# Optimization experiments

Hardware: AMD Instinct MI355X
Metric: run time of the kernel (lower is better)

The kernel has to match this reference:

```python
import math
import jax, jax.numpy as jnp
import numpy as np

NUM_BUCKETS = 32
MAX_DISTANCE = 128
N_HEADS = 16
D_KV = 64


def _relative_position_bucket(rel_pos, num_buckets=NUM_BUCKETS, max_distance=MAX_DISTANCE):
    # bidirectional=True branch of T5's bucketing
    num_buckets = num_buckets // 2
    rel_buckets = (rel_pos > 0).astype(jnp.int32) * num_buckets
    rel_pos = jnp.abs(rel_pos)
    max_exact = num_buckets // 2
    is_small = rel_pos < max_exact
    # safe log (values < max_exact are masked out by is_small)
    rp_f = jnp.maximum(rel_pos, 1).astype(jnp.float32)
    rel_if_large = max_exact + (
        jnp.log(rp_f / max_exact) / math.log(max_distance / max_exact) * (num_buckets - max_exact)
    ).astype(jnp.int32)
    rel_if_large = jnp.minimum(rel_if_large, num_buckets - 1)
    return rel_buckets + jnp.where(is_small, rel_pos, rel_if_large)


def compute_bias(rel_bias_table, q_len, k_len):
    ctx = jnp.arange(q_len)[:, None]
    mem = jnp.arange(k_len)[None, :]
    buckets = _relative_position_bucket(mem - ctx)  # [q, k]
    values = rel_bias_table[buckets]                # [q, k, h]
    return jnp.transpose(values, (2, 0, 1))[None]   # [1, h, q, k]


def setup_inputs() -> dict:
    key = jax.random.key(0)
    k1, k2, k3, k4 = jax.random.split(key, 4)
    d_model = 1024
    return {
        "hidden_states": jax.random.normal(k1, (2, 2048, d_model), jnp.float32),
        "w_qkv": jax.random.normal(k2, (d_model, 3 * N_HEADS * D_KV), jnp.float32) * (d_model ** -0.5),
        "w_o": jax.random.normal(k3, (N_HEADS * D_KV, d_model), jnp.float32) * ((N_HEADS * D_KV) ** -0.5),
        "rel_bias_table": jax.random.normal(k4, (NUM_BUCKETS, N_HEADS), jnp.float32),
    }


def reference(hidden_states, w_qkv, w_o, rel_bias_table):
    b, s, _ = hidden_states.shape
    inner = N_HEADS * D_KV
    qkv = hidden_states @ w_qkv                         # [b, s, 3*inner]
    q, k, v = jnp.split(qkv, [inner, 2 * inner], axis=-1)
    def to_bhsd(x):
        return jnp.transpose(x.reshape(b, s, N_HEADS, D_KV), (0, 2, 1, 3))
    q, k, v = to_bhsd(q), to_bhsd(k), to_bhsd(v)
    scores = jnp.einsum("bhqd,bhkd->bhqk", q, k)        # no 1/sqrt(d) scaling in T5
    position_bias = compute_bias(rel_bias_table, s, s)  # [1, h, q, k]
    scores = scores + position_bias
    attn = jax.nn.softmax(scores.astype(jnp.float32), axis=-1).astype(scores.dtype)
    out = jnp.einsum("bhqk,bhkd->bhqd", attn, v)
    out = jnp.transpose(out, (0, 2, 1, 3)).reshape(b, s, inner)
    attn_output = out @ w_o
    return attn_output, position_bias
```

## Files before the change

kernel.cpp:

```cpp
#include <hip/hip_runtime.h>
#include <hip/hip_bf16.h>
#include <cstdint>
#include <cstddef>

#define S_LEN 2048
#define NH 16
#define DKV 64
#define BATCH 2
#define DMODEL 1024
#define LOG2E 1.4426950408889634f

typedef _Float16 half_t;
typedef __attribute__((ext_vector_type(4))) _Float16 halfx4;
typedef __attribute__((ext_vector_type(8))) _Float16 half8;
typedef __attribute__((ext_vector_type(4))) float floatx4;

__device__ __forceinline__ void load_lds16(const half_t* g, half_t* l) {
  __builtin_amdgcn_global_load_lds((const __attribute__((address_space(1))) void*)g,
                                   (__attribute__((address_space(3))) void*)l, 16, 0, 0);
}

__device__ __forceinline__ int t5_bucket(int delta) {
  int base = (delta > 0) ? 16 : 0;
  int a = delta < 0 ? -delta : delta;
  int n;
  if (a < 8)       n = a;
  else if (a < 12) n = 8;
  else if (a < 16) n = 9;
  else if (a < 23) n = 10;
  else if (a < 32) n = 11;
  else if (a < 46) n = 12;
  else if (a < 64) n = 13;
  else if (a < 91) n = 14;
  else             n = 15;
  return base + n;
}

__global__ __launch_bounds__(256) void bias_kernel(const float* __restrict__ table,
                                                   float* __restrict__ out) {
  int h = blockIdx.x >> 11;
  int q = blockIdx.x & (S_LEN - 1);
  __shared__ float tb[32];
  if (threadIdx.x < 32) tb[threadIdx.x] = table[threadIdx.x * NH + h];
  __syncthreads();
  float* dst = out + (size_t)blockIdx.x * S_LEN;
  int k0 = threadIdx.x * 4;
#pragma unroll
  for (int half = 0; half < 2; half++) {
    int k = k0 + half * 1024;
    float4 v;
    v.x = tb[t5_bucket((k + 0) - q)];
    v.y = tb[t5_bucket((k + 1) - q)];
    v.z = tb[t5_bucket((k + 2) - q)];
    v.w = tb[t5_bucket((k + 3) - q)];
    *(float4*)(dst + k) = v;
  }
}

__global__ __launch_bounds__(256) void cast_f2h(const float* __restrict__ in,
                                                half_t* __restrict__ out) {
  int i = blockIdx.x * 256 + threadIdx.x;
  float4 v = ((const float4*)in)[i];
  halfx4 h;
  h[0] = (half_t)v.x; h[1] = (half_t)v.y; h[2] = (half_t)v.z; h[3] = (half_t)v.w;
  ((halfx4*)out)[i] = h;
}

__global__ __launch_bounds__(256) void transpose_cast(const float* __restrict__ in,
                                                      half_t* __restrict__ out,
                                                      int R, int C) {
  __shared__ float t[32][33];
  int lr = threadIdx.x >> 3;
  int lc = (threadIdx.x & 7) * 4;
  int r0 = blockIdx.y * 32, c0 = blockIdx.x * 32;
  float4 v = *(const float4*)(in + (size_t)(r0 + lr) * C + c0 + lc);
  t[lr][lc + 0] = v.x; t[lr][lc + 1] = v.y; t[lr][lc + 2] = v.z; t[lr][lc + 3] = v.w;
  __syncthreads();
  halfx4 hv;
#pragma unroll
  for (int u = 0; u < 4; u++) hv[u] = (half_t)t[lc + u][lr];
  *(halfx4*)(out + (size_t)(c0 + lr) * R + r0 + lc) = hv;
}

__global__ __launch_bounds__(256) void vtrans(const half_t* __restrict__ V,
                                              half_t* __restrict__ Vt) {
  __shared__ half_t T[64 * 72];
  const int bh = blockIdx.y;
  const int s0 = blockIdx.x * 64;
  const half_t* src = V + ((size_t)bh * S_LEN + s0) * DKV;
  half_t* dst = Vt + (size_t)bh * DKV * S_LEN + s0;
  const int sr = threadIdx.x >> 3;
  const int dc = (threadIdx.x & 7) * 8;
#pragma unroll
  for (int p = 0; p < 2; p++) {
    int s = sr + p * 32;
    half8 v = *(const half8*)(src + (size_t)s * DKV + dc);
#pragma unroll
    for (int u = 0; u < 8; u++) T[(dc + u) * 72 + s] = v[u];
  }
  __syncthreads();
#pragma unroll
  for (int p = 0; p < 2; p++) {
    int d = sr + p * 32;
    half8 v = *(half8*)&T[d * 72 + dc];
    *(half8*)(dst + (size_t)d * S_LEN + dc) = v;
  }
}

template <int MODE>
__global__ __launch_bounds__(256) void hgemm128(const half_t* __restrict__ A,
                                                const half_t* __restrict__ Bt,
                                                float* __restrict__ C,
                                                half_t* __restrict__ Qo,
                                                half_t* __restrict__ Ko,
                                                half_t* __restrict__ Vo,
                                                int M, int N, int K) {
  __shared__ half_t Asl[8 * 512];
  __shared__ half_t Bsl[8 * 512];

  const int tid = threadIdx.x;
  const int w = tid >> 6;
  const int lane = tid & 63;
  const int l15 = lane & 15;
  const int quad = lane >> 4;
  const int wm = w >> 1, wn = w & 1;
  const int m0 = blockIdx.y * 128;
  const int n0 = blockIdx.x * 128;

  floatx4 acc[4][4];
#pragma unroll
  for (int i = 0; i < 4; i++)
#pragma unroll
    for (int j = 0; j < 4; j++) acc[i][j] = (floatx4){0.f, 0.f, 0.f, 0.f};

  const half_t* ga0 = A + (size_t)(m0 + (2 * w + 0) * 16 + l15) * K + quad * 8;
  const half_t* ga1 = A + (size_t)(m0 + (2 * w + 1) * 16 + l15) * K + quad * 8;
  const half_t* gb0 = Bt + (size_t)(n0 + (2 * w + 0) * 16 + l15) * K + quad * 8;
  const half_t* gb1 = Bt + (size_t)(n0 + (2 * w + 1) * 16 + l15) * K + quad * 8;
  half_t* la0 = &Asl[(2 * w + 0) * 512];
  half_t* la1 = &Asl[(2 * w + 1) * 512];
  half_t* lb0 = &Bsl[(2 * w + 0) * 512];
  half_t* lb1 = &Bsl[(2 * w + 1) * 512];

  for (int k0 = 0; k0 < K; k0 += 32) {
    __syncthreads();
    load_lds16(ga0 + k0, la0);
    load_lds16(ga1 + k0, la1);
    load_lds16(gb0 + k0, lb0);
    load_lds16(gb1 + k0, lb1);
    __syncthreads();

    half8 af[4], bf[4];
#pragma unroll
    for (int i = 0; i < 4; i++) af[i] = *(half8*)&Asl[(wm * 4 + i) * 512 + lane * 8];
#pragma unroll
    for (int j = 0; j < 4; j++) bf[j] = *(half8*)&Bsl[(wn * 4 + j) * 512 + lane * 8];
#pragma unroll
    for (int i = 0; i < 4; i++)
#pragma unroll
      for (int j = 0; j < 4; j++)
        acc[i][j] = __builtin_amdgcn_mfma_f32_16x16x32_f16(af[i], bf[j], acc[i][j], 0, 0, 0);
  }

  const int rowbase = m0 + wm * 64;
  const int colbase = n0 + wn * 64;
  if (MODE == 0) {
#pragma unroll
    for (int i = 0; i < 4; i++)
#pragma unroll
      for (int j = 0; j < 4; j++)
#pragma unroll
        for (int r = 0; r < 4; r++)
          C[(size_t)(rowbase + i * 16 + quad * 4 + r) * N + colbase + j * 16 + l15] =
              acc[i][j][r];
  } else {
    const int which = colbase >> 10;
    const int h = (colbase & 1023) >> 6;
    const int b = rowbase >> 11;
    const int s0 = rowbase & (S_LEN - 1);
    const float scale = (which == 0) ? LOG2E : 1.0f;
    half_t* base = ((which == 0) ? Qo : (which == 1) ? Ko : Vo) +
                   (size_t)(b * NH + h) * S_LEN * DKV;
#pragma unroll
    for (int i = 0; i < 4; i++)
#pragma unroll
      for (int j = 0; j < 4; j++)
#pragma unroll
        for (int r = 0; r < 4; r++)
          base[(size_t)(s0 + i * 16 + quad * 4 + r) * DKV + j * 16 + l15] =
              (half_t)(acc[i][j][r] * scale);
  }
}

__global__ __launch_bounds__(512) void attn_fused(const half_t* __restrict__ Q,
                                                  const half_t* __restrict__ K,
                                                  const half_t* __restrict__ Vt,
                                                  const float* __restrict__ table,
                                                  half_t* __restrict__ X) {
  __shared__ half_t Ks[64 * 64];
  __shared__ half_t Vts[64 * 64];
  __shared__ float tb[32];
  __shared__ float badd[184];

  const int tid = threadIdx.x;
  const int w = tid >> 6;
  const int lane = tid & 63;
  const int l15 = lane & 15;
  const int quad = lane >> 4;
  const int bh = blockIdx.y;
  const int h = bh & (NH - 1);
  const int q0w = blockIdx.x * 128 + w * 16;

  if (tid < 32) tb[tid] = table[tid * NH + h] * LOG2E;
  __syncthreads();
  if (tid < 183) badd[tid] = tb[t5_bucket(tid - 91)];
  const float tb_neg = tb[15], tb_pos = tb[31];

  half8 qf[2];
#pragma unroll
  for (int ks = 0; ks < 2; ks++)
    qf[ks] = *(const half8*)(Q + ((size_t)bh * S_LEN + q0w + l15) * DKV +
                             ks * 32 + quad * 8);

  floatx4 o[4];
#pragma unroll
  for (int nb = 0; nb < 4; nb++) o[nb] = (floatx4){0.f, 0.f, 0.f, 0.f};
  float m = -1e30f, l = 0.0f;

  const int jr = tid >> 3;
  const int u = tid & 7;
  const int swu = (u ^ (jr & 7)) * 8;
  const int kv_rd0 = l15 * 64 + ((0 * 4 + quad) ^ (l15 & 7)) * 8;
  const int kv_rd1 = l15 * 64 + ((1 * 4 + quad) ^ (l15 & 7)) * 8;
  const int q2h = quad >> 1, q2l = (quad & 1) * 4;

  const half_t* Kg = K + ((size_t)bh * S_LEN + jr) * DKV + u * 8;
  const half_t* Vg = Vt + ((size_t)bh * DKV + jr) * S_LEN + u * 8;
  int rel = -q0w;

  half8 kreg = *(const half8*)Kg;
  half8 vreg = *(const half8*)Vg;

  for (int it = 0; it < 32; it++, rel += 64) {
    __syncthreads();
    *(half8*)&Ks[jr * 64 + swu] = kreg;
    *(half8*)&Vts[jr * 64 + swu] = vreg;
    __syncthreads();
    if (it < 31) {
      Kg += 64 * DKV;
      Vg += 64;
      kreg = *(const half8*)Kg;
      vreg = *(const half8*)Vg;
    }

    floatx4 s[4];
#pragma unroll
    for (int nb = 0; nb < 4; nb++) {
      s[nb] = (floatx4){0.f, 0.f, 0.f, 0.f};
      s[nb] = __builtin_amdgcn_mfma_f32_16x16x32_f16(
          *(half8*)&Ks[nb * 1024 + kv_rd0], qf[0], s[nb], 0, 0, 0);
      s[nb] = __builtin_amdgcn_mfma_f32_16x16x32_f16(
          *(half8*)&Ks[nb * 1024 + kv_rd1], qf[1], s[nb], 0, 0, 0);
    }

    float cm = fmaxf(fmaxf(fmaxf(s[0][0], s[0][1]), fmaxf(s[0][2], s[0][3])),
                     fmaxf(fmaxf(s[1][0], s[1][1]), fmaxf(s[1][2], s[1][3])));
    cm = fmaxf(cm, fmaxf(fmaxf(fmaxf(s[2][0], s[2][1]), fmaxf(s[2][2], s[2][3])),
                         fmaxf(fmaxf(s[3][0], s[3][1]), fmaxf(s[3][2], s[3][3]))));
    {
      int i = __builtin_amdgcn_ds_swizzle(__float_as_int(cm), 0x401F);
      cm = fmaxf(cm, __int_as_float(i));
      cm = fmaxf(cm, __shfl_xor(cm, 32));
    }
    float mn = fmaxf(m, cm);
    if (!__all(cm <= m)) {
      float al = exp2f(m - mn);
      l *= al;
#pragma unroll
      for (int nb = 0; nb < 4; nb++)
#pragma unroll
        for (int r = 0; r < 4; r++) o[nb][r] *= al;
      m = mn;
    }

    float lsum = 0.0f;
    halfx4 pvb[4];
    if (rel >= 106 || rel <= -154) {
      const float sh = ((rel >= 106) ? tb_pos : tb_neg) - mn;
#pragma unroll
      for (int nb = 0; nb < 4; nb++)
#pragma unroll
        for (int r = 0; r < 4; r++) {
          float p = exp2f(s[nb][r] + sh);
          lsum += p;
          pvb[nb][r] = (half_t)p;
        }
    } else {
      const int db = rel + quad * 4 - l15 + 91;
#pragma unroll
      for (int nb = 0; nb < 4; nb++)
#pragma unroll
        for (int r = 0; r < 4; r++) {
          int idx = db + nb * 16 + r;
          idx = idx < 0 ? 0 : (idx > 182 ? 182 : idx);
          float p = exp2f(s[nb][r] - mn + badd[idx]);
          lsum += p;
          pvb[nb][r] = (half_t)p;
        }
    }
    {
      int i = __builtin_amdgcn_ds_swizzle(__float_as_int(lsum), 0x401F);
      lsum += __int_as_float(i);
      lsum += __shfl_xor(lsum, 32);
    }
    l += lsum;

#pragma unroll
    for (int nb = 0; nb < 4; nb++) {
      const int vrow = (nb * 16 + l15);
      const int vsw = vrow & 7;
#pragma unroll
      for (int kt = 0; kt < 4; kt++) {
        halfx4 vf = *(halfx4*)&Vts[vrow * 64 + ((kt * 2 + q2h) ^ vsw) * 8 + q2l];
        o[nb] = __builtin_amdgcn_mfma_f32_16x16x16f16(vf, pvb[kt], o[nb], 0, 0, 0);
      }
    }
  }

  {
    const float inv = 1.0f / l;
    const int b = bh >> 4;
    half_t* xp = X + (size_t)(b * S_LEN + q0w + l15) * DMODEL + h * DKV;
#pragma unroll
    for (int nb = 0; nb < 4; nb++) {
      halfx4 hv;
#pragma unroll
      for (int r = 0; r < 4; r++) hv[r] = (half_t)(o[nb][r] * inv);
      *(halfx4*)(xp + nb * 16 + quad * 4) = hv;
    }
  }
}

extern "C" void kernel_launch(void* const* d_in, const int* in_sizes, int n_in,
                              void* d_out, int out_size, void* d_ws, size_t ws_size,
                              hipStream_t stream) {
  const float* hidden = (const float*)d_in[0];
  const float* w_qkv = (const float*)d_in[1];
  const float* w_o = (const float*)d_in[2];
  const float* table = (const float*)d_in[3];

  float* attn_out = (float*)d_out;
  float* bias_out = (float*)d_out + 4194304;

  half_t* Ah  = (half_t*)d_ws;
  half_t* Wqt = Ah + 4194304;
  half_t* Wot = Wqt + 3145728;
  half_t* Qh  = Wot + 1048576;
  half_t* Kh  = Qh + 4194304;
  half_t* Vh  = Kh + 4194304;
  half_t* Xh  = Vh + 4194304;
  half_t* Vth = Ah;

  cast_f2h<<<4096, 256, 0, stream>>>(hidden, Ah);
  transpose_cast<<<dim3(3072 / 32, 1024 / 32), 256, 0, stream>>>(w_qkv, Wqt, 1024, 3072);
  transpose_cast<<<dim3(1024 / 32, 1024 / 32), 256, 0, stream>>>(w_o, Wot, 1024, 1024);
  bias_kernel<<<NH * S_LEN, 256, 0, stream>>>(table, bias_out);

  hgemm128<1><<<dim3(3072 / 128, 4096 / 128), 256, 0, stream>>>(
      Ah, Wqt, nullptr, Qh, Kh, Vh, 4096, 3072, 1024);

  vtrans<<<dim3(S_LEN / 64, BATCH * NH), 256, 0, stream>>>(Vh, Vth);

  attn_fused<<<dim3(S_LEN / 128, BATCH * NH), 512, 0, stream>>>(
      Qh, Kh, Vth, table, Xh);

  hgemm128<0><<<dim3(1024 / 128, 4096 / 128), 256, 0, stream>>>(
      Xh, Wot, attn_out, nullptr, nullptr, nullptr, 4096, 1024, 1024);
}
```

Measured before the change: 487.4 us.

## Fold position bias into attention score init, widen GEMM K-step, vectorize stores

The attention kernel now seeds the QK^T MFMA accumulators with the relative-position bias read from a larger table, which removes the clamped bias lookup and add from the exp loop. It also defers the cross-lane row-sum reduction to the end, since per-lane partial sums are rescaled uniformly. The GEMM loads a 64-wide K slice per barrier pair and swaps MFMA operands so each lane writes a contiguous 4-element vector in the epilogue. The bias output kernel uses nontemporal stores. Together these cut per-tile ALU and LDS work, barriers and scattered stores, at the cost of more LDS per GEMM block and slightly different max handling in the capped bias branch.

```diff
diff --git a/kernel.cpp b/kernel.cpp
--- a/kernel.cpp
+++ b/kernel.cpp
@@ -48,12 +48,12 @@
 #pragma unroll
   for (int half = 0; half < 2; half++) {
     int k = k0 + half * 1024;
-    float4 v;
-    v.x = tb[t5_bucket((k + 0) - q)];
-    v.y = tb[t5_bucket((k + 1) - q)];
-    v.z = tb[t5_bucket((k + 2) - q)];
-    v.w = tb[t5_bucket((k + 3) - q)];
-    *(float4*)(dst + k) = v;
+    floatx4 v;
+    v[0] = tb[t5_bucket((k + 0) - q)];
+    v[1] = tb[t5_bucket((k + 1) - q)];
+    v[2] = tb[t5_bucket((k + 2) - q)];
+    v[3] = tb[t5_bucket((k + 3) - q)];
+    __builtin_nontemporal_store(v, (floatx4*)(dst + k));
   }
 }
 
@@ -115,8 +115,8 @@
                                                 half_t* __restrict__ Ko,
                                                 half_t* __restrict__ Vo,
                                                 int M, int N, int K) {
-  __shared__ half_t Asl[8 * 512];
-  __shared__ half_t Bsl[8 * 512];
+  __shared__ half_t Asl[8 * 1024];
+  __shared__ half_t Bsl[8 * 1024];
 
   const int tid = threadIdx.x;
   const int w = tid >> 6;
@@ -137,29 +137,38 @@
   const half_t* ga1 = A + (size_t)(m0 + (2 * w + 1) * 16 + l15) * K + quad * 8;
   const half_t* gb0 = Bt + (size_t)(n0 + (2 * w + 0) * 16 + l15) * K + quad * 8;
   const half_t* gb1 = Bt + (size_t)(n0 + (2 * w + 1) * 16 + l15) * K + quad * 8;
-  half_t* la0 = &Asl[(2 * w + 0) * 512];
-  half_t* la1 = &Asl[(2 * w + 1) * 512];
-  half_t* lb0 = &Bsl[(2 * w + 0) * 512];
-  half_t* lb1 = &Bsl[(2 * w + 1) * 512];
-
-  for (int k0 = 0; k0 < K; k0 += 32) {
+  half_t* la0 = &Asl[(2 * w + 0) * 1024];
+  half_t* la1 = &Asl[(2 * w + 1) * 1024];
+  half_t* lb0 = &Bsl[(2 * w + 0) * 1024];
+  half_t* lb1 = &Bsl[(2 * w + 1) * 1024];
+
+  for (int k0 = 0; k0 < K; k0 += 64) {
     __syncthreads();
-    load_lds16(ga0 + k0, la0);
-    load_lds16(ga1 + k0, la1);
-    load_lds16(gb0 + k0, lb0);
-    load_lds16(gb1 + k0, lb1);
+    load_lds16(ga0 + k0,      la0);
+    load_lds16(ga0 + k0 + 32, la0 + 512);
+    load_lds16(ga1 + k0,      la1);
+    load_lds16(ga1 + k0 + 32, la1 + 512);
+    load_lds16(gb0 + k0,      lb0);
+    load_lds16(gb0 + k0 + 32, lb0 + 512);
+    load_lds16(gb1 + k0,      lb1);
+    load_lds16(gb1 + k0 + 32, lb1 + 512);
     __syncthreads();
 
-    half8 af[4], bf[4];
-#pragma unroll
-    for (int i = 0; i < 4; i++) af[i] = *(half8*)&Asl[(wm * 4 + i) * 512 + lane * 8];
-#pragma unroll
-    for (int j = 0; j < 4; j++) bf[j] = *(half8*)&Bsl[(wn * 4 + j) * 512 + lane * 8];
-#pragma unroll
-    for (int i = 0; i < 4; i++)
+#pragma unroll
+    for (int ks = 0; ks < 2; ks++) {
+      half8 af[4], bf[4];
+#pragma unroll
+      for (int i = 0; i < 4; i++)
+        af[i] = *(half8*)&Asl[(wm * 4 + i) * 1024 + ks * 512 + lane * 8];
 #pragma unroll
       for (int j = 0; j < 4; j++)
-        acc[i][j] = __builtin_amdgcn_mfma_f32_16x16x32_f16(af[i], bf[j], acc[i][j], 0, 0, 0);
+        bf[j] = *(half8*)&Bsl[(wn * 4 + j) * 1024 + ks * 512 + lane * 8];
+#pragma unroll
+      for (int i = 0; i < 4; i++)
+#pragma unroll
+        for (int j = 0; j < 4; j++)
+          acc[i][j] = __builtin_amdgcn_mfma_f32_16x16x32_f16(bf[j], af[i], acc[i][j], 0, 0, 0);
+    }
   }
 
   const int rowbase = m0 + wm * 64;
@@ -169,10 +178,8 @@
     for (int i = 0; i < 4; i++)
 #pragma unroll
       for (int j = 0; j < 4; j++)
-#pragma unroll
-        for (int r = 0; r < 4; r++)
-          C[(size_t)(rowbase + i * 16 + quad * 4 + r) * N + colbase + j * 16 + l15] =
-              acc[i][j][r];
+        *(floatx4*)&C[(size_t)(rowbase + i * 16 + l15) * N + colbase + j * 16 + quad * 4] =
+            acc[i][j];
   } else {
     const int which = colbase >> 10;
     const int h = (colbase & 1023) >> 6;
@@ -184,11 +191,12 @@
 #pragma unroll
     for (int i = 0; i < 4; i++)
 #pragma unroll
-      for (int j = 0; j < 4; j++)
-#pragma unroll
-        for (int r = 0; r < 4; r++)
-          base[(size_t)(s0 + i * 16 + quad * 4 + r) * DKV + j * 16 + l15] =
-              (half_t)(acc[i][j][r] * scale);
+      for (int j = 0; j < 4; j++) {
+        halfx4 hv;
+#pragma unroll
+        for (int r = 0; r < 4; r++) hv[r] = (half_t)(acc[i][j][r] * scale);
+        *(halfx4*)&base[(size_t)(s0 + i * 16 + l15) * DKV + j * 16 + quad * 4] = hv;
+      }
   }
 }
 
@@ -200,7 +208,7 @@
   __shared__ half_t Ks[64 * 64];
   __shared__ half_t Vts[64 * 64];
   __shared__ float tb[32];
-  __shared__ float badd[184];
+  __shared__ float badd2[344];
 
   const int tid = threadIdx.x;
   const int w = tid >> 6;
@@ -213,7 +221,7 @@
 
   if (tid < 32) tb[tid] = table[tid * NH + h] * LOG2E;
   __syncthreads();
-  if (tid < 183) badd[tid] = tb[t5_bucket(tid - 91)];
+  if (tid < 337) badd2[tid] = tb[t5_bucket(tid - 168)];
   const float tb_neg = tb[15], tb_pos = tb[31];
 
   half8 qf[2];
@@ -253,10 +261,23 @@
       vreg = *(const half8*)Vg;
     }
 
+    const bool capped = (rel >= 106 || rel <= -154);
     floatx4 s[4];
+    if (capped) {
+#pragma unroll
+      for (int nb = 0; nb < 4; nb++) s[nb] = (floatx4){0.f, 0.f, 0.f, 0.f};
+    } else {
+      const int db = rel + quad * 4 - l15 + 168;
+#pragma unroll
+      for (int nb = 0; nb < 4; nb++) {
+        s[nb][0] = badd2[db + nb * 16 + 0];
+        s[nb][1] = badd2[db + nb * 16 + 1];
+        s[nb][2] = badd2[db + nb * 16 + 2];
+        s[nb][3] = badd2[db + nb * 16 + 3];
+      }
+    }
 #pragma unroll
     for (int nb = 0; nb < 4; nb++) {
-      s[nb] = (floatx4){0.f, 0.f, 0.f, 0.f};
       s[nb] = __builtin_amdgcn_mfma_f32_16x16x32_f16(
           *(half8*)&Ks[nb * 1024 + kv_rd0], qf[0], s[nb], 0, 0, 0);
       s[nb] = __builtin_amdgcn_mfma_f32_16x16x32_f16(
@@ -272,8 +293,8 @@
       cm = fmaxf(cm, __int_as_float(i));
       cm = fmaxf(cm, __shfl_xor(cm, 32));
     }
-    float mn = fmaxf(m, cm);
     if (!__all(cm <= m)) {
+      float mn = fmaxf(m, cm);
       float al = exp2f(m - mn);
       l *= al;
 #pragma unroll
@@ -285,8 +306,8 @@
 
     float lsum = 0.0f;
     halfx4 pvb[4];
-    if (rel >= 106 || rel <= -154) {
-      const float sh = ((rel >= 106) ? tb_pos : tb_neg) - mn;
+    if (capped) {
+      const float sh = ((rel >= 106) ? tb_pos : tb_neg) - m;
 #pragma unroll
       for (int nb = 0; nb < 4; nb++)
 #pragma unroll
@@ -296,22 +317,14 @@
           pvb[nb][r] = (half_t)p;
         }
     } else {
-      const int db = rel + quad * 4 - l15 + 91;
 #pragma unroll
       for (int nb = 0; nb < 4; nb++)
 #pragma unroll
         for (int r = 0; r < 4; r++) {
-          int idx = db + nb * 16 + r;
-          idx = idx < 0 ? 0 : (idx > 182 ? 182 : idx);
-          float p = exp2f(s[nb][r] - mn + badd[idx]);
+          float p = exp2f(s[nb][r] - m);
           lsum += p;
           pvb[nb][r] = (half_t)p;
         }
-    }
-    {
-      int i = __builtin_amdgcn_ds_swizzle(__float_as_int(lsum), 0x401F);
-      lsum += __int_as_float(i);
-      lsum += __shfl_xor(lsum, 32);
     }
     l += lsum;
 
@@ -328,6 +341,9 @@
   }
 
   {
+    int i = __builtin_amdgcn_ds_swizzle(__float_as_int(l), 0x401F);
+    l += __int_as_float(i);
+    l += __shfl_xor(l, 32);
     const float inv = 1.0f / l;
     const int b = bh >> 4;
     half_t* xp = X + (size_t)(b * S_LEN + q0w + l15) * DMODEL + h * DKV;
```

After: 477.5 us. 2.0% less time.
